# Optimization experiments

Measured on AMD Instinct MI355X. Metric: run time of the kernel, lower is better.

Reference implementation:

```python
import jax, jax.numpy as jnp
import numpy as np

IN_FEATURES = 4096
OUT_FEATURES = 11008


def setup_inputs() -> dict:
    key = jax.random.key(0)
    k1, k2, k3 = jax.random.split(key, 3)
    x = jax.random.normal(k1, (4, 2048, IN_FEATURES), dtype=jnp.float32)
    # int8-valued weights stored as int32 (range [-127, 127] emulated via [0,127) here)
    weight_quantized = jax.random.randint(k2, (OUT_FEATURES, IN_FEATURES), 0, 127, dtype=jnp.int32)
    weight_scale = jax.random.uniform(k3, (OUT_FEATURES,), dtype=jnp.float32) * 0.01 + 1e-4
    return {"x": x, "weight_quantized": weight_quantized, "weight_scale": weight_scale}


def reference(x, weight_quantized, weight_scale):
    # Dequantize: per-output-channel scale, then dense GEMM (F.linear semantics: y = x @ W^T)
    weight_fp = weight_quantized.astype(x.dtype) * weight_scale[:, None].astype(x.dtype)
    # x: [B, S, in], weight_fp: [out, in] -> [B, S, out]
    return jnp.einsum('bsi,oi->bso', x, weight_fp)
```

## Files before the change

kernel.cpp:

```cpp
#include <hip/hip_runtime.h>
#include <stdint.h>
#include <stddef.h>

#define M_DIM 8192
#define N_DIM 11008
#define K_DIM 4096

typedef __attribute__((ext_vector_type(8))) __bf16 bf16x8;
typedef __attribute__((ext_vector_type(4))) float f32x4;

typedef const __attribute__((address_space(1))) void gvoid;
typedef __attribute__((address_space(3))) void lvoid;

__device__ __forceinline__ void async16(const void* g, void* l) {
  __builtin_amdgcn_global_load_lds((gvoid*)g, (lvoid*)l, 16, 0, 0);
}

__device__ __forceinline__ unsigned short f2bf(float f) {
  unsigned u = __float_as_uint(f);
  u += 0x7fffu + ((u >> 16) & 1u);
  return (unsigned short)(u >> 16);
}


__global__ __launch_bounds__(256) void cvt_x_kernel(const float* __restrict__ x,
                                                    unsigned short* __restrict__ xw) {
  size_t i = ((size_t)blockIdx.x * 256 + threadIdx.x) * 4;
  float4 v = *(const float4*)(x + i);
  ushort4 o;
  o.x = f2bf(v.x); o.y = f2bf(v.y); o.z = f2bf(v.z); o.w = f2bf(v.w);
  *(ushort4*)(xw + i) = o;
}

__global__ __launch_bounds__(256) void cvt_w_kernel(const int* __restrict__ wq,
                                                    unsigned short* __restrict__ ww) {
  size_t i = ((size_t)blockIdx.x * 256 + threadIdx.x) * 4;
  int4 v = *(const int4*)(wq + i);
  ushort4 o;
  o.x = f2bf((float)v.x); o.y = f2bf((float)v.y);
  o.z = f2bf((float)v.z); o.w = f2bf((float)v.w);
  *(ushort4*)(ww + i) = o;
}


__global__ __launch_bounds__(256) void gemm_bf16(const unsigned short* __restrict__ xw,
                                                 const unsigned short* __restrict__ ww,
                                                 const float* __restrict__ scale,
                                                 float* __restrict__ out) {
  __shared__ unsigned short As[128 * 32];
  __shared__ unsigned short Bs[128 * 32];

  const int tid = threadIdx.x;
  const int w = tid >> 6;
  const int l = tid & 63;
  const int n0 = blockIdx.x * 128;
  const int m0 = blockIdx.y * 128;

  const int srow = w * 16 + (l >> 2);
  const int scol = (l & 3) * 8;
  const unsigned short* ga = xw + (size_t)(m0 + srow) * K_DIM + scol;
  const unsigned short* gb = ww + (size_t)(n0 + srow) * K_DIM + scol;
  unsigned short* lA0 = &As[w * 512];
  unsigned short* lA1 = &As[2048 + w * 512];
  unsigned short* lB0 = &Bs[w * 512];
  unsigned short* lB1 = &Bs[2048 + w * 512];

  const int wm = w >> 1, wn = w & 1;
  const int fm = l & 15;
  const int q = l >> 4;
  const unsigned short* pA = &As[(wm * 64 + fm) * 32 + q * 8];
  const unsigned short* pB = &Bs[(wn * 64 + fm) * 32 + q * 8];

  f32x4 acc[4][4];
#pragma unroll
  for (int i = 0; i < 4; i++)
#pragma unroll
    for (int j = 0; j < 4; j++) acc[i][j] = {0.f, 0.f, 0.f, 0.f};

  for (int kk = 0; kk < K_DIM; kk += 32) {
    __syncthreads();
    async16(ga + kk, lA0);
    async16(ga + kk + (size_t)64 * K_DIM, lA1);
    async16(gb + kk, lB0);
    async16(gb + kk + (size_t)64 * K_DIM, lB1);
    __syncthreads();

    bf16x8 af[4], bf[4];
#pragma unroll
    for (int i = 0; i < 4; i++) af[i] = *(const bf16x8*)(pA + i * 16 * 32);
#pragma unroll
    for (int j = 0; j < 4; j++) bf[j] = *(const bf16x8*)(pB + j * 16 * 32);
#pragma unroll
    for (int i = 0; i < 4; i++)
#pragma unroll
      for (int j = 0; j < 4; j++)
        acc[i][j] = __builtin_amdgcn_mfma_f32_16x16x32_bf16(af[i], bf[j], acc[i][j], 0, 0, 0);
  }

  float sc[4];
  const int baseN = n0 + wn * 64 + fm;
#pragma unroll
  for (int j = 0; j < 4; j++) sc[j] = scale[baseN + j * 16];
#pragma unroll
  for (int i = 0; i < 4; i++) {
#pragma unroll
    for (int r = 0; r < 4; r++) {
      size_t row = (size_t)(m0 + wm * 64 + i * 16 + q * 4 + r);
      float* po = out + row * N_DIM + baseN;
#pragma unroll
      for (int j = 0; j < 4; j++) po[j * 16] = acc[i][j][r] * sc[j];
    }
  }
}


__global__ __launch_bounds__(256) void gemm_fused(const float* __restrict__ x,
                                                  const int* __restrict__ wq,
                                                  const float* __restrict__ scale,
                                                  float* __restrict__ out) {
  __shared__ unsigned short As[128 * 32];
  __shared__ unsigned short Bs[128 * 32];

  const int tid = threadIdx.x;
  const int w = tid >> 6, l = tid & 63;
  const int n0 = blockIdx.x * 128;
  const int m0 = blockIdx.y * 128;

  const int srow = tid >> 2;
  const int scol = (tid & 3) * 8;

  const int wm = w >> 1, wn = w & 1;
  const int fm = l & 15, q = l >> 4;
  const unsigned short* pA = &As[(wm * 64 + fm) * 32 + q * 8];
  const unsigned short* pB = &Bs[(wn * 64 + fm) * 32 + q * 8];

  f32x4 acc[4][4];
#pragma unroll
  for (int i = 0; i < 4; i++)
#pragma unroll
    for (int j = 0; j < 4; j++) acc[i][j] = {0.f, 0.f, 0.f, 0.f};

  for (int kk = 0; kk < K_DIM; kk += 32) {
    __syncthreads();
#pragma unroll
    for (int h = 0; h < 2; h++) {
      int row = h * 64 + srow;
      const float* pa = x + (size_t)(m0 + row) * K_DIM + kk + scol;
      float4 a0 = *(const float4*)pa;
      float4 a1 = *(const float4*)(pa + 4);
      union { unsigned short us[8]; bf16x8 v; } ua;
      ua.us[0] = f2bf(a0.x); ua.us[1] = f2bf(a0.y); ua.us[2] = f2bf(a0.z); ua.us[3] = f2bf(a0.w);
      ua.us[4] = f2bf(a1.x); ua.us[5] = f2bf(a1.y); ua.us[6] = f2bf(a1.z); ua.us[7] = f2bf(a1.w);
      *(bf16x8*)&As[row * 32 + scol] = ua.v;

      const int* pb = wq + (size_t)(n0 + row) * K_DIM + kk + scol;
      int4 b0 = *(const int4*)pb;
      int4 b1 = *(const int4*)(pb + 4);
      union { unsigned short us[8]; bf16x8 v; } ub;
      ub.us[0] = f2bf((float)b0.x); ub.us[1] = f2bf((float)b0.y);
      ub.us[2] = f2bf((float)b0.z); ub.us[3] = f2bf((float)b0.w);
      ub.us[4] = f2bf((float)b1.x); ub.us[5] = f2bf((float)b1.y);
      ub.us[6] = f2bf((float)b1.z); ub.us[7] = f2bf((float)b1.w);
      *(bf16x8*)&Bs[row * 32 + scol] = ub.v;
    }
    __syncthreads();

    bf16x8 af[4], bf[4];
#pragma unroll
    for (int i = 0; i < 4; i++) af[i] = *(const bf16x8*)(pA + i * 16 * 32);
#pragma unroll
    for (int j = 0; j < 4; j++) bf[j] = *(const bf16x8*)(pB + j * 16 * 32);
#pragma unroll
    for (int i = 0; i < 4; i++)
#pragma unroll
      for (int j = 0; j < 4; j++)
        acc[i][j] = __builtin_amdgcn_mfma_f32_16x16x32_bf16(af[i], bf[j], acc[i][j], 0, 0, 0);
  }

  float sc[4];
  const int baseN = n0 + wn * 64 + fm;
#pragma unroll
  for (int j = 0; j < 4; j++) sc[j] = scale[baseN + j * 16];
#pragma unroll
  for (int i = 0; i < 4; i++) {
#pragma unroll
    for (int r = 0; r < 4; r++) {
      size_t row = (size_t)(m0 + wm * 64 + i * 16 + q * 4 + r);
      float* po = out + row * N_DIM + baseN;
#pragma unroll
      for (int j = 0; j < 4; j++) po[j * 16] = acc[i][j][r] * sc[j];
    }
  }
}

extern "C" void kernel_launch(void* const* d_in, const int* in_sizes, int n_in,
                              void* d_out, int out_size, void* d_ws, size_t ws_size,
                              hipStream_t stream) {
  const float* x = (const float*)d_in[0];
  const int* wq = (const int*)d_in[1];
  const float* sc = (const float*)d_in[2];
  float* out = (float*)d_out;

  const size_t xE = (size_t)M_DIM * K_DIM;
  const size_t wE = (size_t)N_DIM * K_DIM;
  const size_t need = (xE + wE) * sizeof(unsigned short);

  dim3 grid(N_DIM / 128, M_DIM / 128);

  if (ws_size >= need) {
    unsigned short* xw = (unsigned short*)d_ws;
    unsigned short* ww = xw + xE;
    cvt_x_kernel<<<(unsigned)(xE / 1024), 256, 0, stream>>>(x, xw);
    cvt_w_kernel<<<(unsigned)(wE / 1024), 256, 0, stream>>>(wq, ww);
    gemm_bf16<<<grid, 256, 0, stream>>>(xw, ww, sc, out);
  } else {
    gemm_fused<<<grid, 256, 0, stream>>>(x, wq, sc, out);
  }
}
```

Measured before the change: 1.462 ms.

## Replace bf16 GEMM with 256x256-tile, 8-wave, double-buffered pipelined kernel

Swaps the simple 128x128 single-buffered GEMM for a 256x256 tile kernel with 512 threads, a 64-wide K step and double-buffered LDS loaded by async global-to-LDS copies. Each phase interleaves the prefetch of the next stage with MFMA work under explicit barriers, wait counts and setprio, uses an XOR swizzle to avoid LDS bank conflicts, and remaps block indices for L2 locality. It aims to hide global memory latency and raise MFMA utilisation. In exchange it uses 128 KB of dynamic LDS, more registers, and hand-tuned scheduling that is fragile.

```diff
diff --git a/kernel.cpp b/kernel.cpp
--- a/kernel.cpp
+++ b/kernel.cpp
@@ -43,72 +43,155 @@
 }
 
 
-__global__ __launch_bounds__(256) void gemm_bf16(const unsigned short* __restrict__ xw,
-                                                 const unsigned short* __restrict__ ww,
-                                                 const float* __restrict__ scale,
-                                                 float* __restrict__ out) {
-  __shared__ unsigned short As[128 * 32];
-  __shared__ unsigned short Bs[128 * 32];
+#define PH_MID                                            \
+  __builtin_amdgcn_sched_barrier(0);                      \
+  __builtin_amdgcn_s_barrier();                           \
+  asm volatile("s_waitcnt lgkmcnt(0)" ::: "memory");      \
+  __builtin_amdgcn_sched_barrier(0);                      \
+  __builtin_amdgcn_s_setprio(1)
+
+#define PH_END                                            \
+  __builtin_amdgcn_s_setprio(0);                          \
+  __builtin_amdgcn_sched_barrier(0);                      \
+  __builtin_amdgcn_s_barrier()
+
+#define PH_END_VM                                         \
+  __builtin_amdgcn_s_setprio(0);                          \
+  asm volatile("s_waitcnt vmcnt(4)" ::: "memory");        \
+  __builtin_amdgcn_sched_barrier(0);                      \
+  __builtin_amdgcn_s_barrier()
+
+#define LD8(p, off) (*(const bf16x8*)((p) + (off)))
+
+#define RD_A(PA0, PA1, IOFF)                                   \
+  _Pragma("unroll") for (int ii = 0; ii < 4; ii++) {           \
+    aR[ii][0] = LD8(PA0, ((IOFF) + ii) * 1024);                \
+    aR[ii][1] = LD8(PA1, ((IOFF) + ii) * 1024);                \
+  }
+
+#define RD_B(BR, PB0, PB1, JOFF)                               \
+  _Pragma("unroll") for (int jj = 0; jj < 2; jj++) {           \
+    BR[jj][0] = LD8(PB0, ((JOFF) + jj) * 1024);                \
+    BR[jj][1] = LD8(PB1, ((JOFF) + jj) * 1024);                \
+  }
+
+#define MFQ(IB, JB, BR)                                                         \
+  _Pragma("unroll") for (int ii = 0; ii < 4; ii++)                              \
+  _Pragma("unroll") for (int jj = 0; jj < 2; jj++)                              \
+  _Pragma("unroll") for (int ss = 0; ss < 2; ss++)                              \
+    acc[(IB) + ii][(JB) + jj] = __builtin_amdgcn_mfma_f32_16x16x32_bf16(        \
+        aR[ii][ss], BR[jj][ss], acc[(IB) + ii][(JB) + jj], 0, 0, 0)
+
+#define STG(g, s, h, u, kk)                                                     \
+  async16((g) + (size_t)((h) * 128 + (u) * 64) * K_DIM + (kk),                  \
+          (s) + ((h) * 128 + (u) * 64) * 64)
+
+__global__ __launch_bounds__(512, 2) void gemm8(const unsigned short* __restrict__ xw,
+                                                const unsigned short* __restrict__ ww,
+                                                const float* __restrict__ scale,
+                                                float* __restrict__ out) {
+  extern __shared__ unsigned short smem[];
 
   const int tid = threadIdx.x;
-  const int w = tid >> 6;
+  const int v = tid >> 6;
   const int l = tid & 63;
-  const int n0 = blockIdx.x * 128;
-  const int m0 = blockIdx.y * 128;
-
-  const int srow = w * 16 + (l >> 2);
-  const int scol = (l & 3) * 8;
-  const unsigned short* ga = xw + (size_t)(m0 + srow) * K_DIM + scol;
-  const unsigned short* gb = ww + (size_t)(n0 + srow) * K_DIM + scol;
-  unsigned short* lA0 = &As[w * 512];
-  unsigned short* lA1 = &As[2048 + w * 512];
-  unsigned short* lB0 = &Bs[w * 512];
-  unsigned short* lB1 = &Bs[2048 + w * 512];
-
-  const int wm = w >> 1, wn = w & 1;
-  const int fm = l & 15;
-  const int q = l >> 4;
-  const unsigned short* pA = &As[(wm * 64 + fm) * 32 + q * 8];
-  const unsigned short* pB = &Bs[(wn * 64 + fm) * 32 + q * 8];
-
-  f32x4 acc[4][4];
-#pragma unroll
-  for (int i = 0; i < 4; i++)
+  const int wm = v >> 2, wn = v & 3;
+  const int fm = l & 15, q = l >> 4;
+
+  const int flat = blockIdx.x;
+  const int swz = (flat & 7) * 172 + (flat >> 3);
+  const int m0 = (swz & 31) * 256;
+  const int n0 = (swz >> 5) * 256;
+
+  const int sr = l >> 3;
+  const int scn = (l & 7) ^ sr;
+  const unsigned short* gA = xw + (size_t)(m0 + v * 8 + sr) * K_DIM + scn * 8;
+  const unsigned short* gB = ww + (size_t)(n0 + v * 8 + sr) * K_DIM + scn * 8;
+  unsigned short* const sA0 = smem + (v * 8) * 64;
+  unsigned short* const sA1 = smem + 16384 + (v * 8) * 64;
+  unsigned short* const sB0 = smem + 32768 + (v * 8) * 64;
+  unsigned short* const sB1 = smem + 49152 + (v * 8) * 64;
+
+  const int ca = q ^ (fm & 7);
+  const unsigned short* const pA0 = smem + (wm * 128 + fm) * 64 + ca * 8;
+  const unsigned short* const pA1 = smem + (wm * 128 + fm) * 64 + (ca ^ 4) * 8;
+  const unsigned short* const pB0 = smem + 32768 + (wn * 64 + fm) * 64 + ca * 8;
+  const unsigned short* const pB1 = smem + 32768 + (wn * 64 + fm) * 64 + (ca ^ 4) * 8;
+  const unsigned short* const pA0o = pA0 + 16384;
+  const unsigned short* const pA1o = pA1 + 16384;
+  const unsigned short* const pB0o = pB0 + 16384;
+  const unsigned short* const pB1o = pB1 + 16384;
+
+  f32x4 acc[8][4];
+#pragma unroll
+  for (int i = 0; i < 8; i++)
 #pragma unroll
     for (int j = 0; j < 4; j++) acc[i][j] = {0.f, 0.f, 0.f, 0.f};
 
-  for (int kk = 0; kk < K_DIM; kk += 32) {
-    __syncthreads();
-    async16(ga + kk, lA0);
-    async16(ga + kk + (size_t)64 * K_DIM, lA1);
-    async16(gb + kk, lB0);
-    async16(gb + kk + (size_t)64 * K_DIM, lB1);
-    __syncthreads();
-
-    bf16x8 af[4], bf[4];
-#pragma unroll
-    for (int i = 0; i < 4; i++) af[i] = *(const bf16x8*)(pA + i * 16 * 32);
-#pragma unroll
-    for (int j = 0; j < 4; j++) bf[j] = *(const bf16x8*)(pB + j * 16 * 32);
-#pragma unroll
-    for (int i = 0; i < 4; i++)
-#pragma unroll
-      for (int j = 0; j < 4; j++)
-        acc[i][j] = __builtin_amdgcn_mfma_f32_16x16x32_bf16(af[i], bf[j], acc[i][j], 0, 0, 0);
-  }
-
-  float sc[4];
+  bf16x8 aR[4][2], b0R[2][2], b1R[2][2];
+
+  STG(gA, sA0, 0, 0, 0); STG(gA, sA0, 0, 1, 0);
+  STG(gA, sA0, 1, 0, 0); STG(gA, sA0, 1, 1, 0);
+  STG(gB, sB0, 0, 0, 0); STG(gB, sB0, 0, 1, 0);
+  STG(gB, sB0, 1, 0, 0); STG(gB, sB0, 1, 1, 0);
+  STG(gA, sA1, 0, 0, 64); STG(gA, sA1, 0, 1, 64);
+  STG(gA, sA1, 1, 0, 64); STG(gA, sA1, 1, 1, 64);
+  asm volatile("s_waitcnt vmcnt(4)" ::: "memory");
+  __builtin_amdgcn_sched_barrier(0);
+  __builtin_amdgcn_s_barrier();
+
+  for (int it2 = 0; it2 < K_DIM / 128; ++it2) {
+    const int ka = it2 * 128;
+    const int k1 = ka + 64;
+    int k2 = ka + 128; if (k2 > K_DIM - 64) k2 = K_DIM - 64;
+    int k3 = ka + 192; if (k3 > K_DIM - 64) k3 = K_DIM - 64;
+
+    RD_A(pA0, pA1, 0);
+    RD_B(b0R, pB0, pB1, 0);
+    STG(gB, sB1, 0, 0, k1); STG(gB, sB1, 0, 1, k1);
+    PH_MID; MFQ(0, 0, b0R); PH_END;
+
+    RD_B(b1R, pB0, pB1, 2);
+    STG(gB, sB1, 1, 0, k1); STG(gB, sB1, 1, 1, k1);
+    PH_MID; MFQ(0, 2, b1R); PH_END;
+
+    RD_A(pA0, pA1, 4);
+    STG(gB, sB0, 0, 0, k2); STG(gB, sB0, 0, 1, k2);
+    PH_MID; MFQ(4, 0, b0R); PH_END;
+
+    STG(gA, sA0, 0, 0, k2); STG(gA, sA0, 0, 1, k2);
+    PH_MID; MFQ(4, 2, b1R); PH_END_VM;
+
+    RD_A(pA0o, pA1o, 0);
+    RD_B(b0R, pB0o, pB1o, 0);
+    STG(gA, sA0, 1, 0, k2); STG(gA, sA0, 1, 1, k2);
+    PH_MID; MFQ(0, 0, b0R); PH_END;
+
+    RD_B(b1R, pB0o, pB1o, 2);
+    STG(gB, sB0, 1, 0, k2); STG(gB, sB0, 1, 1, k2);
+    PH_MID; MFQ(0, 2, b1R); PH_END;
+
+    RD_A(pA0o, pA1o, 4);
+    __builtin_amdgcn_sched_barrier(0);
+    STG(gA, sA1, 0, 0, k3); STG(gA, sA1, 0, 1, k3);
+    PH_MID; MFQ(4, 0, b0R); PH_END;
+
+    STG(gA, sA1, 1, 0, k3); STG(gA, sA1, 1, 1, k3);
+    PH_MID; MFQ(4, 2, b1R); PH_END_VM;
+  }
+
+  float sc4[4];
   const int baseN = n0 + wn * 64 + fm;
 #pragma unroll
-  for (int j = 0; j < 4; j++) sc[j] = scale[baseN + j * 16];
-#pragma unroll
-  for (int i = 0; i < 4; i++) {
+  for (int j = 0; j < 4; j++) sc4[j] = scale[baseN + j * 16];
+#pragma unroll
+  for (int i = 0; i < 8; i++) {
 #pragma unroll
     for (int r = 0; r < 4; r++) {
-      size_t row = (size_t)(m0 + wm * 64 + i * 16 + q * 4 + r);
+      size_t row = (size_t)(m0 + wm * 128 + i * 16 + q * 4 + r);
       float* po = out + row * N_DIM + baseN;
 #pragma unroll
-      for (int j = 0; j < 4; j++) po[j * 16] = acc[i][j][r] * sc[j];
+      for (int j = 0; j < 4; j++) po[j * 16] = acc[i][j][r] * sc4[j];
     }
   }
 }
@@ -148,20 +231,20 @@
       const float* pa = x + (size_t)(m0 + row) * K_DIM + kk + scol;
       float4 a0 = *(const float4*)pa;
       float4 a1 = *(const float4*)(pa + 4);
-      union { unsigned short us[8]; bf16x8 v; } ua;
+      union { unsigned short us[8]; bf16x8 vv; } ua;
       ua.us[0] = f2bf(a0.x); ua.us[1] = f2bf(a0.y); ua.us[2] = f2bf(a0.z); ua.us[3] = f2bf(a0.w);
       ua.us[4] = f2bf(a1.x); ua.us[5] = f2bf(a1.y); ua.us[6] = f2bf(a1.z); ua.us[7] = f2bf(a1.w);
-      *(bf16x8*)&As[row * 32 + scol] = ua.v;
+      *(bf16x8*)&As[row * 32 + scol] = ua.vv;
 
       const int* pb = wq + (size_t)(n0 + row) * K_DIM + kk + scol;
       int4 b0 = *(const int4*)pb;
       int4 b1 = *(const int4*)(pb + 4);
-      union { unsigned short us[8]; bf16x8 v; } ub;
+      union { unsigned short us[8]; bf16x8 vv; } ub;
       ub.us[0] = f2bf((float)b0.x); ub.us[1] = f2bf((float)b0.y);
       ub.us[2] = f2bf((float)b0.z); ub.us[3] = f2bf((float)b0.w);
       ub.us[4] = f2bf((float)b1.x); ub.us[5] = f2bf((float)b1.y);
       ub.us[6] = f2bf((float)b1.z); ub.us[7] = f2bf((float)b1.w);
-      *(bf16x8*)&Bs[row * 32 + scol] = ub.v;
+      *(bf16x8*)&Bs[row * 32 + scol] = ub.vv;
     }
     __syncthreads();
 
@@ -205,15 +288,19 @@
   const size_t wE = (size_t)N_DIM * K_DIM;
   const size_t need = (xE + wE) * sizeof(unsigned short);
 
-  dim3 grid(N_DIM / 128, M_DIM / 128);
-
   if (ws_size >= need) {
+    static bool attr_set = false;
+    if (!attr_set) {
+      (void)hipFuncSetAttribute(reinterpret_cast<const void*>(gemm8),
+                                hipFuncAttributeMaxDynamicSharedMemorySize, 131072);
+      attr_set = true;
+    }
     unsigned short* xw = (unsigned short*)d_ws;
     unsigned short* ww = xw + xE;
     cvt_x_kernel<<<(unsigned)(xE / 1024), 256, 0, stream>>>(x, xw);
     cvt_w_kernel<<<(unsigned)(wE / 1024), 256, 0, stream>>>(wq, ww);
-    gemm_bf16<<<grid, 256, 0, stream>>>(xw, ww, sc, out);
+    gemm8<<<dim3((M_DIM / 256) * (N_DIM / 256)), dim3(512), 131072, stream>>>(xw, ww, sc, out);
   } else {
-    gemm_fused<<<grid, 256, 0, stream>>>(x, wq, sc, out);
-  }
-}
+    gemm_fused<<<dim3(N_DIM / 128, M_DIM / 128), 256, 0, stream>>>(x, wq, sc, out);
+  }
+}
```

Result: faster. 1.179 ms (-19.4%).
